# Kernel optimization log

Measured on AMD Instinct MI355X. Metric: run time of the kernel, lower is better.

The kernel has to match this reference:

```python
import jax, jax.numpy as jnp
import numpy as np

GRID = 128      # voxel grid extent per axis
NUM_BATCH = 4
N_PER = 25000   # points per scene (unique voxels)
C = 128
K = 32          # number of classes in probs
HEADS = 8
SCALE = 1.0


def setup_inputs() -> dict:
    key = jax.random.key(0)
    ks = jax.random.split(key, 12)
    N = NUM_BATCH * N_PER
    # unique voxel coordinates per scene (submanifold conv assumes no duplicate sites)
    coords_list = []
    for b in range(NUM_BATCH):
        flat = jax.random.permutation(jax.random.fold_in(ks[0], b), GRID ** 3)[:N_PER]
        xyz = jnp.stack([flat // (GRID * GRID), (flat // GRID) % GRID, flat % GRID], axis=1)
        bcol = jnp.full((N_PER, 1), b)
        coords_list.append(jnp.concatenate([bcol, xyz], axis=1))
    coords = jnp.concatenate(coords_list, axis=0).astype(jnp.int32)  # [N,4] = (b,x,y,z)
    feats = jax.random.normal(ks[1], (N, C), jnp.float32)
    probs = jax.random.normal(ks[2], (N, K), jnp.float32)
    conv_w = jax.random.normal(ks[3], (27, C, C), jnp.float32) * (1.0 / np.sqrt(27 * C))
    bn_gamma = 1.0 + 0.1 * jax.random.normal(ks[4], (C,), jnp.float32)
    bn_beta = 0.1 * jax.random.normal(ks[5], (C,), jnp.float32)
    in_proj_w = jax.random.normal(ks[6], (3 * C, C), jnp.float32) / np.sqrt(C)
    in_proj_b = 0.01 * jax.random.normal(ks[7], (3 * C,), jnp.float32)
    out_proj_w = jax.random.normal(ks[8], (C, C), jnp.float32) / np.sqrt(C)
    out_proj_b = 0.01 * jax.random.normal(ks[9], (C,), jnp.float32)
    bottleneck_w = jax.random.normal(ks[10], (C, 2 * C), jnp.float32) / np.sqrt(2 * C)
    return {"feats": feats, "probs": probs, "conv_w": conv_w, "bn_gamma": bn_gamma,
            "bn_beta": bn_beta, "in_proj_w": in_proj_w, "in_proj_b": in_proj_b,
            "out_proj_w": out_proj_w, "out_proj_b": out_proj_b,
            "bottleneck_w": bottleneck_w, "coords": coords, "batch_size": NUM_BATCH}


def _subm_conv3x3(feats, coords, conv_w, batch_size):
    """Submanifold 3x3x3 sparse conv: outputs only at active sites, gathering active neighbors."""
    N = feats.shape[0]
    b, xyz = coords[:, 0], coords[:, 1:]
    grid = jnp.full((batch_size, GRID, GRID, GRID), -1, jnp.int32)
    grid = grid.at[b, xyz[:, 0], xyz[:, 1], xyz[:, 2]].set(jnp.arange(N, dtype=jnp.int32))
    out = jnp.zeros((N, conv_w.shape[-1]), feats.dtype)
    kidx = 0
    for dx in (-1, 0, 1):
        for dy in (-1, 0, 1):
            for dz in (-1, 0, 1):
                nb = xyz + jnp.array([dx, dy, dz], jnp.int32)
                inb = jnp.all((nb >= 0) & (nb < GRID), axis=1)
                nbc = jnp.clip(nb, 0, GRID - 1)
                j = grid[b, nbc[:, 0], nbc[:, 1], nbc[:, 2]]
                ok = inb & (j >= 0)
                g = jnp.where(ok[:, None], feats[jnp.maximum(j, 0)], 0.0)
                out = out + g @ conv_w[kidx]
                kidx += 1
    return out


def _forward(feats, probs, conv_w, bn_gamma, bn_beta, in_proj_w, in_proj_b,
             out_proj_w, out_proj_b, bottleneck_w, coords, batch_size):
    N, Cc = feats.shape
    dh = Cc // HEADS
    b = coords[:, 0]
    # transform_input: SubMConv3d -> BatchNorm1d (batch stats) -> ReLU
    x = _subm_conv3x3(feats, coords, conv_w, batch_size)
    mu = jnp.mean(x, axis=0)
    var = jnp.var(x, axis=0)
    x = jax.nn.relu((x - mu) * jax.lax.rsqrt(var + 1e-5) * bn_gamma + bn_beta)
    # SpatialGatherModule: per-scene softmax over points, soft-weighted context [B,K,C]
    m = b[None, :] == jnp.arange(batch_size, dtype=b.dtype)[:, None]          # [B,N]
    neg = jnp.finfo(x.dtype).min
    z = jnp.where(m[:, :, None], (SCALE * probs)[None], neg)                  # [B,N,K]
    w = jax.nn.softmax(z, axis=1)
    ctx = jnp.einsum('bnk,nc->bkc', w, x)                                     # [B,K,C]
    # per-scene MultiheadAttention (unbatched): query = points, key/value = context
    Wq, Wk, Wv = in_proj_w[:Cc], in_proj_w[Cc:2 * Cc], in_proj_w[2 * Cc:]
    bq, bk, bv = in_proj_b[:Cc], in_proj_b[Cc:2 * Cc], in_proj_b[2 * Cc:]
    q = ((x @ Wq.T + bq) * (dh ** -0.5)).reshape(N, HEADS, dh)
    kh = (ctx @ Wk.T + bk).reshape(batch_size, -1, HEADS, dh)
    vh = (ctx @ Wv.T + bv).reshape(batch_size, -1, HEADS, dh)
    scores = jnp.einsum('nhd,bkhd->nbhk', q, kh)
    scores = scores[jnp.arange(N), b]                                         # [N,H,K] pick own scene
    attn = jax.nn.softmax(scores, axis=-1)
    o = jnp.einsum('nhk,bkhd->nbhd', attn, vh)[jnp.arange(N), b]              # [N,H,dh]
    attn_out = o.reshape(N, Cc) @ out_proj_w.T + out_proj_b
    # torch code aliases feats with inputs.features, so the in-place scatter makes
    # both halves of the concat equal to attn_out (literal forward semantics)
    y = jnp.concatenate([attn_out, attn_out], axis=1) @ bottleneck_w.T
    return y


def reference(feats, probs, conv_w, bn_gamma, bn_beta, in_proj_w, in_proj_b,
              out_proj_w, out_proj_b, bottleneck_w, coords, batch_size):
    return _forward(feats, probs, conv_w, bn_gamma, bn_beta, in_proj_w, in_proj_b,
                    out_proj_w, out_proj_b, bottleneck_w, coords, batch_size)
```

## Files before the change

### kernel.cpp

```cpp
#include <hip/hip_runtime.h>
#include <hip/hip_bf16.h>

typedef __attribute__((ext_vector_type(8))) short short8;
typedef __attribute__((ext_vector_type(4))) float floatx4;

#define NB 4
#define GRIDD 128
#define GRID3 (128*128*128)
#define C 128
#define KSLOT 32
#define CTX_BPB 256
#define DEN_BLK 1024
#define STAT_BLK 1024
#define PCAP 8192
#define PREP_BLKS 2048

static __device__ __forceinline__ unsigned short f2bf(float f){
  unsigned u = __builtin_bit_cast(unsigned, f);
  unsigned r = (u + 0x7FFFu + ((u >> 16) & 1u)) >> 16;
  return (unsigned short)r;
}
static __device__ __forceinline__ float bf2f(unsigned short h){
  unsigned u = ((unsigned)h) << 16;
  return __builtin_bit_cast(float, u);
}

__global__ void prepk(const float* __restrict__ feats, const float* __restrict__ convw,
                      const float* __restrict__ inw, const int* __restrict__ coords,
                      const float* __restrict__ bw, const float* __restrict__ outw,
                      const float* __restrict__ outb,
                      unsigned short* __restrict__ Fb, unsigned short* __restrict__ Wt,
                      unsigned short* __restrict__ Wq, unsigned short* __restrict__ WkvT,
                      int* __restrict__ gh, unsigned short* __restrict__ W2b,
                      float* __restrict__ b2, long total1)
{
  const int t = threadIdx.x;
  if (blockIdx.x >= PREP_BLKS){
    __shared__ float wcf[128];
    __shared__ float red[128];
    const int o = blockIdx.x - PREP_BLKS;
    if (t < 128){
      const float w_i = bw[(size_t)o*256 + t] + bw[(size_t)o*256 + 128 + t];
      wcf[t] = w_i;
      red[t] = w_i * outb[t];
    }
    __syncthreads();
    if (t < 128){
      float acc = 0.f;
      #pragma unroll 8
      for (int j = 0; j < 128; j++) acc = fmaf(wcf[j], outw[j*128 + t], acc);
      W2b[o*128 + t] = f2bf(acc);
    }
    for (int s = 64; s > 0; s >>= 1){
      if (t < s) red[t] += red[t + s];
      __syncthreads();
    }
    if (t == 0) b2[o] = red[0];
    return;
  }
  const long stride = (long)PREP_BLKS * blockDim.x;
  const long i0 = (long)blockIdx.x * blockDim.x + t;
  const long q4 = total1 >> 2;
  const float4* f4 = reinterpret_cast<const float4*>(feats);
  ushort4* fb4 = reinterpret_cast<ushort4*>(Fb);
  for (long i = i0; i < q4; i += stride){
    const float4 v = f4[i];
    ushort4 o; o.x = f2bf(v.x); o.y = f2bf(v.y); o.z = f2bf(v.z); o.w = f2bf(v.w);
    fb4[i] = o;
  }
  for (long i = i0; i < 27L*C*C; i += stride){
    long k = i >> 14; long r = (i >> 7) & 127; long c = i & 127;
    Wt[i] = f2bf(convw[(k << 14) + (c << 7) + r]);
  }
  for (long i = i0; i < C*C; i += stride) Wq[i] = f2bf(inw[i]);
  for (long i = i0; i < 2L*C*C; i += stride){
    long which = i >> 14, rem = i & 16383, ii = rem >> 7, cout = rem & 127;
    WkvT[i] = f2bf(inw[((1 + which) << 14) + (cout << 7) + ii]);
  }
  const long nsites = total1 >> 7;
  for (long i = i0; i < nsites; i += stride){
    const int4 cr = *reinterpret_cast<const int4*>(coords + i * 4);
    gh[(((cr.x*GRIDD + cr.y)*GRIDD + cr.z)*GRIDD) + cr.w] = (int)i;
  }
}

__global__ __launch_bounds__(256) void pairk(const int* __restrict__ coords,
                                             const int* __restrict__ gh,
                                             int2* __restrict__ pairs,
                                             int* __restrict__ gcnt, int N){
  __shared__ int wcnt[4][27];
  __shared__ int woff[4][27];
  const int t = threadIdx.x, wave = t >> 6, lane = t & 63;
  const int p = blockIdx.x * 256 + t;
  const bool active = p < N;
  int4 cr = make_int4(0, 0, 0, 0);
  if (active) cr = *reinterpret_cast<const int4*>(coords + (size_t)p * 4);
  const int b = cr.x, x = cr.y, y = cr.z, z = cr.w;
  int jl[27];
  #pragma unroll
  for (int k = 0; k < 27; k++){
    jl[k] = -1;
    if (k == 13) continue;
    if (active){
      const int dx = k / 9 - 1, dy = (k / 3) % 3 - 1, dz = k % 3 - 1;
      const int nx = x + dx, ny = y + dy, nz = z + dz;
      if (((unsigned)nx < 128u) & ((unsigned)ny < 128u) & ((unsigned)nz < 128u)){
        const int gi = ((((b << 7) + nx) << 7) + ny) * GRIDD + nz;
        const int jj = gh[gi];
        if ((unsigned)jj < (unsigned)N){
          const int4 cj = *reinterpret_cast<const int4*>(coords + (size_t)jj * 4);
          if (cj.x == b && cj.y == nx && cj.z == ny && cj.w == nz) jl[k] = jj;
        }
      }
    }
  }
  #pragma unroll
  for (int k = 0; k < 27; k++){
    const unsigned long long m = __ballot(jl[k] >= 0);
    if (lane == 0) wcnt[wave][k] = (int)__popcll(m);
  }
  __syncthreads();
  if (t < 27){
    const int c0 = wcnt[0][t], c1 = wcnt[1][t], c2 = wcnt[2][t], c3 = wcnt[3][t];
    const int tot = c0 + c1 + c2 + c3;
    int gb = 0;
    if (t != 13 && tot > 0) gb = atomicAdd(&gcnt[t], tot);
    woff[0][t] = gb;
    woff[1][t] = gb + c0;
    woff[2][t] = gb + c0 + c1;
    woff[3][t] = gb + c0 + c1 + c2;
  }
  __syncthreads();
  const unsigned long long ltm = ((unsigned long long)1 << lane) - 1;
  #pragma unroll
  for (int k = 0; k < 27; k++){
    if (k == 13) continue;
    const unsigned long long m = __ballot(jl[k] >= 0);
    if (jl[k] >= 0){
      const int slot = woff[wave][k] + (int)__popcll(m & ltm);
      if (slot < PCAP) pairs[(size_t)k * PCAP + slot] = make_int2(p, jl[k]);
    }
  }
}

__global__ __launch_bounds__(256) void scatk(
    const unsigned short* __restrict__ F, const unsigned short* __restrict__ Wt,
    const int2* __restrict__ pairs, const int* __restrict__ gcnt,
    float* __restrict__ X, int N)
{
  __shared__ unsigned short wl[128 * 136];
  const int k = (blockIdx.x < 13) ? blockIdx.x : blockIdx.x + 1;
  const int t = threadIdx.x;
  const unsigned short* wg = Wt + (size_t)k * C * C;
  for (int idx = t; idx < 128 * 16; idx += 256){
    const int row = idx >> 4, seg = idx & 15;
    *reinterpret_cast<short8*>(&wl[row * 136 + seg * 8]) =
        *reinterpret_cast<const short8*>(wg + row * 128 + seg * 8);
  }
  __syncthreads();
  const int cnt = min(gcnt[k], PCAP);
  const int nch = (cnt + 15) >> 4;
  const int wave = t >> 6, lane = t & 63, lo = lane & 15, hi = lane >> 4;
  for (int c = blockIdx.y * 4 + wave; c < nch; c += 32 * 4){
    const int pidx = c * 16 + lo;
    const bool pv = pidx < cnt;
    const int2 pr = pv ? pairs[(size_t)k * PCAP + pidx] : make_int2(0, 0);
    const unsigned short* frow = F + (size_t)pr.y * C;
    short8 a[4];
    #pragma unroll
    for (int kc = 0; kc < 4; kc++){
      a[kc] = *reinterpret_cast<const short8*>(frow + kc * 32 + hi * 8);
      if (!pv) a[kc] = (short8){0,0,0,0,0,0,0,0};
    }
    floatx4 acc[8];
    #pragma unroll
    for (int i = 0; i < 8; i++) acc[i] = (floatx4){0.f,0.f,0.f,0.f};
    #pragma unroll
    for (int kc = 0; kc < 4; kc++){
      const int koff = kc * 32 + hi * 8;
      #pragma unroll
      for (int ct = 0; ct < 8; ct++){
        const short8 b = *reinterpret_cast<const short8*>(&wl[(ct*16 + lo) * 136 + koff]);
        acc[ct] = __builtin_amdgcn_mfma_f32_16x16x32_bf16(a[kc], b, acc[ct], 0, 0, 0);
      }
    }
    #pragma unroll
    for (int i2 = 0; i2 < 4; i2++){
      const int src = hi * 4 + i2;
      const int row = __shfl(pr.x, src);
      if (c * 16 + src < cnt){
        #pragma unroll
        for (int ct = 0; ct < 8; ct++)
          atomicAdd(&X[(size_t)row * C + ct * 16 + lo], acc[ct][i2]);
      }
    }
  }
}

__global__ __launch_bounds__(256) void sdk(const float* __restrict__ X,
                                           const float* __restrict__ probs,
                                           const int* __restrict__ coords,
                                           float* __restrict__ spgs,
                                           float* __restrict__ dpart, int N){
  __shared__ float ls[256][4];
  __shared__ float lq[256][4];
  const int t = threadIdx.x;
  if (blockIdx.x < STAT_BLK){
    const int blk = blockIdx.x;
    const int c4 = t & 31, rg = t >> 5;
    float s0=0.f,s1=0.f,s2=0.f,s3=0.f, q0=0.f,q1=0.f,q2=0.f,q3=0.f;
    for (int r = blk * 8 + rg; r < N; r += STAT_BLK * 8){
      const float4 v = *reinterpret_cast<const float4*>(X + (size_t)r * C + c4 * 4);
      s0 += v.x; s1 += v.y; s2 += v.z; s3 += v.w;
      q0 = fmaf(v.x, v.x, q0); q1 = fmaf(v.y, v.y, q1);
      q2 = fmaf(v.z, v.z, q2); q3 = fmaf(v.w, v.w, q3);
    }
    ls[t][0]=s0; ls[t][1]=s1; ls[t][2]=s2; ls[t][3]=s3;
    lq[t][0]=q0; lq[t][1]=q1; lq[t][2]=q2; lq[t][3]=q3;
    __syncthreads();
    if (t < 32){
      float as[4]={0.f,0.f,0.f,0.f}, aq[4]={0.f,0.f,0.f,0.f};
      #pragma unroll
      for (int g = 0; g < 8; g++){
        #pragma unroll
        for (int j = 0; j < 4; j++){ as[j] += ls[g*32 + t][j]; aq[j] += lq[g*32 + t][j]; }
      }
      #pragma unroll
      for (int j = 0; j < 4; j++){
        spgs[(size_t)blk * 256 + t*4 + j] = as[j];
        spgs[(size_t)blk * 256 + 128 + t*4 + j] = aq[j];
      }
    }
  } else {
    const int blk = blockIdx.x - STAT_BLK;
    const int k = t & 31, rh = t >> 5;
    float a0 = 0.f, a1 = 0.f, a2 = 0.f, a3 = 0.f;
    for (int r = blk * 8 + rh; r < N; r += DEN_BLK * 8){
      const int b = coords[(size_t)r * 4];
      const float e = __expf(probs[(size_t)r * 32 + k]);
      a0 += (b == 0) ? e : 0.f;
      a1 += (b == 1) ? e : 0.f;
      a2 += (b == 2) ? e : 0.f;
      a3 += (b == 3) ? e : 0.f;
    }
    float (*dls)[128] = reinterpret_cast<float (*)[128]>(&ls[0][0]);
    dls[rh][0*32 + k] = a0; dls[rh][1*32 + k] = a1;
    dls[rh][2*32 + k] = a2; dls[rh][3*32 + k] = a3;
    __syncthreads();
    if (t < 128){
      float s = 0.f;
      #pragma unroll
      for (int j = 0; j < 8; j++) s += dls[j][t];
      dpart[(size_t)blk * 128 + t] = s;
    }
  }
}

__global__ __launch_bounds__(128) void reduk(const float* __restrict__ pgs,
                                             const float* __restrict__ dpart,
                                             float* __restrict__ gsum,
                                             float* __restrict__ gsq,
                                             float* __restrict__ denom){
  const int which = blockIdx.x, slice = blockIdx.y, t = threadIdx.x;
  float s = 0.f;
  if (which < 2){
    const float* src = pgs + which * 128 + t;
    for (int j = slice; j < STAT_BLK; j += 8) s += src[(size_t)j * 256];
    atomicAdd((which ? gsq : gsum) + t, s);
  } else {
    const float* src = dpart + t;
    for (int j = slice; j < DEN_BLK; j += 8) s += src[(size_t)j * 128];
    atomicAdd(denom + t, s);
  }
}

__global__ void finalizek(const float* __restrict__ sums, const float* __restrict__ sumsq,
                          const float* __restrict__ gamma, const float* __restrict__ beta,
                          const float* __restrict__ denom,
                          float* __restrict__ scalev, float* __restrict__ shiftv,
                          float* __restrict__ invden, int N){
  const int t = threadIdx.x;
  const float invN = 1.f / (float)N;
  const float mu = sums[t] * invN;
  const float var = sumsq[t] * invN - mu * mu;
  const float sc = gamma[t] * rsqrtf(var + 1e-5f);
  scalev[t] = sc;
  shiftv[t] = beta[t] - mu * sc;
  invden[t] = 1.f / denom[t];
}

__global__ __launch_bounds__(256) void ctx2k(const float* __restrict__ Xm,
                                             const float* __restrict__ probs,
                                             const float* __restrict__ scalev,
                                             const float* __restrict__ shiftv,
                                             float* __restrict__ pbuf,
                                             unsigned short* __restrict__ xb, int NPER){
  __shared__ float xL[32 * 128];
  __shared__ float pe[32 * 32];
  __shared__ float red[2 * KSLOT * C];
  __shared__ float scL[128], shL[128];
  const int blk = blockIdx.x;
  const int b = blk >> 8, j = blk & 255;
  const int rows = (NPER + CTX_BPB - 1) / CTX_BPB;
  const int r0 = j * rows;
  const int r1 = min(r0 + rows, NPER);
  const int t = threadIdx.x, c = t & 127, rh = t >> 7;
  if (t < 128){ scL[t] = scalev[t]; shL[t] = shiftv[t]; }
  __syncthreads();
  const float sc = scL[c], sh = shL[c];
  float acc[KSLOT];
  #pragma unroll
  for (int k = 0; k < KSLOT; k++) acc[k] = 0.f;

  const int wr = t >> 3;
  const int wc = (t & 7) * 16;

  for (int base = r0; base < r1; base += 32){
    __syncthreads();
    #pragma unroll
    for (int i = 0; i < 4; i++){
      const int idx = i * 256 + t;
      const int r = idx >> 5, c4 = idx & 31;
      const int rr = base + r;
      float4 v = make_float4(0.f, 0.f, 0.f, 0.f);
      if (rr < r1) v = *reinterpret_cast<const float4*>(Xm + ((size_t)b * NPER + rr) * C + c4 * 4);
      *reinterpret_cast<float4*>(&xL[r * 128 + c4 * 4]) = v;
    }
    {
      const int r = t >> 3, k4 = t & 7;
      const int rr = base + r;
      float4 v = make_float4(0.f, 0.f, 0.f, 0.f);
      if (rr < r1){
        const float4 pv = *reinterpret_cast<const float4*>(probs + ((size_t)b * NPER + rr) * 32 + k4 * 4);
        v.x = __expf(pv.x); v.y = __expf(pv.y); v.z = __expf(pv.z); v.w = __expf(pv.w);
      }
      *reinterpret_cast<float4*>(&pe[r * 32 + k4 * 4]) = v;
    }
    __syncthreads();
    {
      const int rr = base + wr;
      if (rr < r1){
        short8 o0, o1;
        #pragma unroll
        for (int jj = 0; jj < 8; jj++){
          o0[jj] = (short)f2bf(fmaxf(fmaf(xL[wr * 128 + wc + jj], scL[wc + jj], shL[wc + jj]), 0.f));
          o1[jj] = (short)f2bf(fmaxf(fmaf(xL[wr * 128 + wc + 8 + jj], scL[wc + 8 + jj], shL[wc + 8 + jj]), 0.f));
        }
        unsigned short* xp = xb + ((size_t)b * NPER + rr) * C + wc;
        *reinterpret_cast<short8*>(xp) = o0;
        *reinterpret_cast<short8*>(xp + 8) = o1;
      }
    }
    const int rend = min(32, r1 - base);
    for (int r = rh; r < rend; r += 2){
      const float xv = fmaxf(fmaf(xL[r * 128 + c], sc, sh), 0.f);
      const float4* wrp = reinterpret_cast<const float4*>(&pe[r * 32]);
      #pragma unroll
      for (int kq = 0; kq < 8; kq++){
        const float4 w4 = wrp[kq];
        acc[kq*4+0] = fmaf(w4.x, xv, acc[kq*4+0]);
        acc[kq*4+1] = fmaf(w4.y, xv, acc[kq*4+1]);
        acc[kq*4+2] = fmaf(w4.z, xv, acc[kq*4+2]);
        acc[kq*4+3] = fmaf(w4.w, xv, acc[kq*4+3]);
      }
    }
  }
  __syncthreads();
  #pragma unroll
  for (int k = 0; k < KSLOT; k++) red[(rh * KSLOT + k) * C + c] = acc[k];
  __syncthreads();
  float* dst = pbuf + (size_t)blk * KSLOT * C;
  for (int i = t; i < KSLOT * C; i += 256) dst[i] = red[i] + red[KSLOT * C + i];
}

__global__ __launch_bounds__(256) void kvk(const float* __restrict__ pbuf,
                                           const float* __restrict__ invden,
                                           const unsigned short* __restrict__ WkvT,
                                           const float* __restrict__ inb,
                                           float* __restrict__ kh, float* __restrict__ vh){
  __shared__ float rowp[2][C];
  __shared__ float row[C];
  const int bk = blockIdx.x;
  const int b = bk >> 5, k = bk & 31;
  const int t = threadIdx.x, c = t & 127, jh = t >> 7;
  float s = 0.f;
  for (int j = jh; j < CTX_BPB; j += 2)
    s += pbuf[((size_t)(b * CTX_BPB + j) * KSLOT + k) * C + c];
  rowp[jh][c] = s;
  __syncthreads();
  if (t < C) row[t] = (rowp[0][t] + rowp[1][t]) * invden[b * KSLOT + k];
  __syncthreads();
  const int which = t >> 7;
  const unsigned short* W = WkvT + (size_t)which * C * C;
  float acc = inb[(1 + which) * C + c];
  #pragma unroll 8
  for (int i = 0; i < C; i++) acc = fmaf(row[i], bf2f(W[i * C + c]), acc);
  (which ? vh : kh)[(size_t)bk * C + c] = acc;
}

__global__ __launch_bounds__(256) void gemm128(
    const unsigned short* __restrict__ A, const unsigned short* __restrict__ W,
    const float* __restrict__ bias, float scale,
    float* __restrict__ outF, unsigned short* __restrict__ outB, int N)
{
  const int tid = threadIdx.x;
  const int wave = tid >> 6, lane = tid & 63;
  const int rbase = blockIdx.x * 64 + (wave >> 1) * 32;
  const int cbase = (wave & 1) * 64;
  const int lo = lane & 15, hi = lane >> 4;
  floatx4 acc[2][4];
  #pragma unroll
  for (int rt = 0; rt < 2; rt++)
    #pragma unroll
    for (int ct = 0; ct < 4; ct++) acc[rt][ct] = (floatx4){0.f,0.f,0.f,0.f};
  const int m0 = rbase + lo, m1 = rbase + 16 + lo;
  const int m0c = m0 < N ? m0 : N - 1;
  const int m1c = m1 < N ? m1 : N - 1;
  #pragma unroll
  for (int kc = 0; kc < 4; kc++){
    const int koff = kc * 32 + hi * 8;
    const short8 a0 = *reinterpret_cast<const short8*>(A + (size_t)m0c * C + koff);
    const short8 a1 = *reinterpret_cast<const short8*>(A + (size_t)m1c * C + koff);
    #pragma unroll
    for (int ct = 0; ct < 4; ct++){
      const int n = cbase + ct * 16 + lo;
      const short8 b = *reinterpret_cast<const short8*>(W + (size_t)n * C + koff);
      acc[0][ct] = __builtin_amdgcn_mfma_f32_16x16x32_bf16(b, a0, acc[0][ct], 0, 0, 0);
      acc[1][ct] = __builtin_amdgcn_mfma_f32_16x16x32_bf16(b, a1, acc[1][ct], 0, 0, 0);
    }
  }
  #pragma unroll
  for (int rt = 0; rt < 2; rt++){
    const int row = rbase + rt * 16 + lo;
    if (row < N){
      #pragma unroll
      for (int ct = 0; ct < 4; ct++){
        const int col = cbase + ct * 16 + hi * 4;
        float4 bv = make_float4(0.f, 0.f, 0.f, 0.f);
        if (bias) bv = *reinterpret_cast<const float4*>(bias + col);
        float4 v;
        v.x = (acc[rt][ct][0] + bv.x) * scale;
        v.y = (acc[rt][ct][1] + bv.y) * scale;
        v.z = (acc[rt][ct][2] + bv.z) * scale;
        v.w = (acc[rt][ct][3] + bv.w) * scale;
        if (outF) *reinterpret_cast<float4*>(outF + (size_t)row * C + col) = v;
        if (outB){
          ushort4 u;
          u.x = f2bf(v.x); u.y = f2bf(v.y); u.z = f2bf(v.z); u.w = f2bf(v.w);
          *reinterpret_cast<ushort4*>(outB + (size_t)row * C + col) = u;
        }
      }
    }
  }
}

__global__ __launch_bounds__(256) void attn5k(const unsigned short* __restrict__ qb,
                                              const float* __restrict__ kh,
                                              const float* __restrict__ vh,
                                              unsigned short* __restrict__ ob, int NPER){
  __shared__ float khL[KSLOT * C];
  __shared__ float vhL[KSLOT * C];
  const int t = threadIdx.x;
  const int b = blockIdx.y;
  const int n0 = blockIdx.x * 64;
  {
    const float4* ks = reinterpret_cast<const float4*>(kh + (size_t)b * KSLOT * C);
    const float4* vs = reinterpret_cast<const float4*>(vh + (size_t)b * KSLOT * C);
    float4* kd = reinterpret_cast<float4*>(khL);
    float4* vd = reinterpret_cast<float4*>(vhL);
    #pragma unroll
    for (int i = 0; i < 4; i++){ kd[i * 256 + t] = ks[i * 256 + t]; vd[i * 256 + t] = vs[i * 256 + t]; }
  }
  __syncthreads();
  const int h = t >> 5, p = t & 31;
  const int na = n0 + p, nb = n0 + 32 + p;
  const int nac = na < NPER ? na : NPER - 1;
  const int nbc = nb < NPER ? nb : NPER - 1;
  float qa[16], qc[16];
  {
    const short8* qpa = reinterpret_cast<const short8*>(qb + ((size_t)b * NPER + nac) * C + h * 16);
    const short8* qpb = reinterpret_cast<const short8*>(qb + ((size_t)b * NPER + nbc) * C + h * 16);
    const short8 a0 = qpa[0], a1 = qpa[1];
    const short8 b0 = qpb[0], b1 = qpb[1];
    #pragma unroll
    for (int i = 0; i < 8; i++){
      qa[i]     = bf2f((unsigned short)a0[i]);
      qa[8 + i] = bf2f((unsigned short)a1[i]);
      qc[i]     = bf2f((unsigned short)b0[i]);
      qc[8 + i] = bf2f((unsigned short)b1[i]);
    }
  }
  float ma = -3.0e38f, mb = -3.0e38f;
  float sa = 0.f, sb = 0.f;
  float oa[16], oc[16];
  #pragma unroll
  for (int i = 0; i < 16; i++){ oa[i] = 0.f; oc[i] = 0.f; }
  for (int tau = 0; tau < 4; tau++){
    float va[8], vb[8];
    #pragma unroll
    for (int kk = 0; kk < 8; kk++){
      const int k = tau * 8 + kk;
      const float4* kp = reinterpret_cast<const float4*>(&khL[k * C + h * 16]);
      const float4 k0 = kp[0], k1 = kp[1], k2 = kp[2], k3 = kp[3];
      float x, y;
      x = qa[0] * k0.x;            y = qc[0] * k0.x;
      x = fmaf(qa[1],  k0.y, x);   y = fmaf(qc[1],  k0.y, y);
      x = fmaf(qa[2],  k0.z, x);   y = fmaf(qc[2],  k0.z, y);
      x = fmaf(qa[3],  k0.w, x);   y = fmaf(qc[3],  k0.w, y);
      x = fmaf(qa[4],  k1.x, x);   y = fmaf(qc[4],  k1.x, y);
      x = fmaf(qa[5],  k1.y, x);   y = fmaf(qc[5],  k1.y, y);
      x = fmaf(qa[6],  k1.z, x);   y = fmaf(qc[6],  k1.z, y);
      x = fmaf(qa[7],  k1.w, x);   y = fmaf(qc[7],  k1.w, y);
      x = fmaf(qa[8],  k2.x, x);   y = fmaf(qc[8],  k2.x, y);
      x = fmaf(qa[9],  k2.y, x);   y = fmaf(qc[9],  k2.y, y);
      x = fmaf(qa[10], k2.z, x);   y = fmaf(qc[10], k2.z, y);
      x = fmaf(qa[11], k2.w, x);   y = fmaf(qc[11], k2.w, y);
      x = fmaf(qa[12], k3.x, x);   y = fmaf(qc[12], k3.x, y);
      x = fmaf(qa[13], k3.y, x);   y = fmaf(qc[13], k3.y, y);
      x = fmaf(qa[14], k3.z, x);   y = fmaf(qc[14], k3.z, y);
      x = fmaf(qa[15], k3.w, x);   y = fmaf(qc[15], k3.w, y);
      va[kk] = x; vb[kk] = y;
    }
    float tma = va[0], tmb = vb[0];
    #pragma unroll
    for (int kk = 1; kk < 8; kk++){ tma = fmaxf(tma, va[kk]); tmb = fmaxf(tmb, vb[kk]); }
    const float ma2 = fmaxf(ma, tma), mb2 = fmaxf(mb, tmb);
    const float fa = __expf(ma - ma2), fb = __expf(mb - mb2);
    ma = ma2; mb = mb2;
    sa *= fa; sb *= fb;
    #pragma unroll
    for (int i = 0; i < 16; i++){ oa[i] *= fa; oc[i] *= fb; }
    #pragma unroll
    for (int kk = 0; kk < 8; kk++){
      const float ea = __expf(va[kk] - ma);
      const float eb = __expf(vb[kk] - mb);
      va[kk] = ea; vb[kk] = eb;
      sa += ea; sb += eb;
    }
    #pragma unroll
    for (int kk = 0; kk < 8; kk++){
      const int k = tau * 8 + kk;
      const float4* vp = reinterpret_cast<const float4*>(&vhL[k * C + h * 16]);
      const float4 v0 = vp[0], v1 = vp[1], v2 = vp[2], v3 = vp[3];
      const float wa = va[kk], wb = vb[kk];
      oa[0]  = fmaf(wa, v0.x, oa[0]);   oc[0]  = fmaf(wb, v0.x, oc[0]);
      oa[1]  = fmaf(wa, v0.y, oa[1]);   oc[1]  = fmaf(wb, v0.y, oc[1]);
      oa[2]  = fmaf(wa, v0.z, oa[2]);   oc[2]  = fmaf(wb, v0.z, oc[2]);
      oa[3]  = fmaf(wa, v0.w, oa[3]);   oc[3]  = fmaf(wb, v0.w, oc[3]);
      oa[4]  = fmaf(wa, v1.x, oa[4]);   oc[4]  = fmaf(wb, v1.x, oc[4]);
      oa[5]  = fmaf(wa, v1.y, oa[5]);   oc[5]  = fmaf(wb, v1.y, oc[5]);
      oa[6]  = fmaf(wa, v1.z, oa[6]);   oc[6]  = fmaf(wb, v1.z, oc[6]);
      oa[7]  = fmaf(wa, v1.w, oa[7]);   oc[7]  = fmaf(wb, v1.w, oc[7]);
      oa[8]  = fmaf(wa, v2.x, oa[8]);   oc[8]  = fmaf(wb, v2.x, oc[8]);
      oa[9]  = fmaf(wa, v2.y, oa[9]);   oc[9]  = fmaf(wb, v2.y, oc[9]);
      oa[10] = fmaf(wa, v2.z, oa[10]);  oc[10] = fmaf(wb, v2.z, oc[10]);
      oa[11] = fmaf(wa, v2.w, oa[11]);  oc[11] = fmaf(wb, v2.w, oc[11]);
      oa[12] = fmaf(wa, v3.x, oa[12]);  oc[12] = fmaf(wb, v3.x, oc[12]);
      oa[13] = fmaf(wa, v3.y, oa[13]);  oc[13] = fmaf(wb, v3.y, oc[13]);
      oa[14] = fmaf(wa, v3.z, oa[14]);  oc[14] = fmaf(wb, v3.z, oc[14]);
      oa[15] = fmaf(wa, v3.w, oa[15]);  oc[15] = fmaf(wb, v3.w, oc[15]);
    }
  }
  const float inva = 1.f / sa, invb = 1.f / sb;
  if (na < NPER){
    short8 s0, s1;
    #pragma unroll
    for (int i = 0; i < 8; i++){
      s0[i] = (short)f2bf(oa[i] * inva);
      s1[i] = (short)f2bf(oa[8 + i] * inva);
    }
    unsigned short* op = ob + ((size_t)b * NPER + na) * C + h * 16;
    *reinterpret_cast<short8*>(op) = s0;
    *reinterpret_cast<short8*>(op + 8) = s1;
  }
  if (nb < NPER){
    short8 s0, s1;
    #pragma unroll
    for (int i = 0; i < 8; i++){
      s0[i] = (short)f2bf(oc[i] * invb);
      s1[i] = (short)f2bf(oc[8 + i] * invb);
    }
    unsigned short* op = ob + ((size_t)b * NPER + nb) * C + h * 16;
    *reinterpret_cast<short8*>(op) = s0;
    *reinterpret_cast<short8*>(op + 8) = s1;
  }
}

extern "C" void kernel_launch(void* const* d_in, const int* in_sizes, int n_in,
                              void* d_out, int out_size, void* d_ws, size_t ws_size,
                              hipStream_t stream){
  const float* feats  = (const float*)d_in[0];
  const float* probs  = (const float*)d_in[1];
  const float* convw  = (const float*)d_in[2];
  const float* gamma  = (const float*)d_in[3];
  const float* beta   = (const float*)d_in[4];
  const float* inw    = (const float*)d_in[5];
  const float* inb    = (const float*)d_in[6];
  const float* outw   = (const float*)d_in[7];
  const float* outb   = (const float*)d_in[8];
  const float* bw     = (const float*)d_in[9];
  const int*   coords = (const int*)d_in[10];
  const int N = in_sizes[0] / C;
  const int NPER = N / NB;
  const int NBLK = (N + 63) / 64;

  char* ws = (char*)d_ws;
  size_t off = 0;
  auto alloc = [&](size_t bytes) -> char* {
    char* r = ws + off; off += (bytes + 255) & ~(size_t)255; return r;
  };
  int* grid_h            = (int*)alloc((size_t)NB * GRID3 * 4);
  unsigned short* featsb = (unsigned short*)alloc((size_t)N * C * 2);
  unsigned short* convwt = (unsigned short*)alloc((size_t)27 * C * C * 2);
  unsigned short* wq     = (unsigned short*)alloc((size_t)C * C * 2);
  unsigned short* wkvT   = (unsigned short*)alloc((size_t)2 * C * C * 2);
  unsigned short* w2b    = (unsigned short*)alloc((size_t)C * C * 2);
  float* b2              = (float*)alloc(512);
  float* xconv           = (float*)alloc((size_t)N * C * 4);
  unsigned short* qb     = (unsigned short*)alloc((size_t)N * C * 2);
  unsigned short* xb     = (unsigned short*)alloc((size_t)N * C * 2);
  int2* pairs            = (int2*)alloc((size_t)27 * PCAP * 8);
  float* spgs            = (float*)alloc((size_t)STAT_BLK * 256 * 4);
  float* dpart           = (float*)alloc((size_t)DEN_BLK * 128 * 4);
  float* zero_base       = (float*)alloc((size_t)512 * 4);
  float* gsum   = zero_base;
  float* gsq    = zero_base + 128;
  float* denom  = zero_base + 256;
  int*   gcnt   = (int*)(zero_base + 384);
  float* invden = (float*)alloc(512);
  float* scalev = (float*)alloc(512);
  float* shiftv = (float*)alloc(512);
  float* kh     = (float*)alloc((size_t)NB * KSLOT * C * 4);
  float* vh     = (float*)alloc((size_t)NB * KSLOT * C * 4);
  float* pbuf = (float*)grid_h;
  unsigned short* o_bf = featsb;

  (void)hipMemsetAsync(zero_base, 0, (size_t)512 * 4, stream);
  prepk<<<PREP_BLKS + 128, 256, 0, stream>>>(feats, convw, inw, coords, bw, outw, outb,
                                             featsb, convwt, wq, wkvT, grid_h, w2b, b2,
                                             (long)N * C);
  pairk<<<(N + 255) / 256, 256, 0, stream>>>(coords, grid_h, pairs, gcnt, N);
  gemm128<<<NBLK, 256, 0, stream>>>(featsb, convwt + 13 * C * C, nullptr, 1.f, xconv, nullptr, N);
  scatk<<<dim3(26, 32), 256, 0, stream>>>(featsb, convwt, pairs, gcnt, xconv, N);
  sdk<<<STAT_BLK + DEN_BLK, 256, 0, stream>>>(xconv, probs, coords, spgs, dpart, N);
  {
    dim3 rg(3, 8);
    reduk<<<rg, 128, 0, stream>>>(spgs, dpart, gsum, gsq, denom);
  }
  finalizek<<<1, 128, 0, stream>>>(gsum, gsq, gamma, beta, denom, scalev, shiftv, invden, N);
  ctx2k<<<NB * CTX_BPB, 256, 0, stream>>>(xconv, probs, scalev, shiftv, pbuf, xb, NPER);
  kvk<<<NB * KSLOT, 256, 0, stream>>>(pbuf, invden, wkvT, inb, kh, vh);
  gemm128<<<NBLK, 256, 0, stream>>>(xb, wq, inb, 0.25f, nullptr, qb, N);
  dim3 agrid((NPER + 63) / 64, NB);
  attn5k<<<agrid, 256, 0, stream>>>(qb, kh, vh, o_bf, NPER);
  gemm128<<<NBLK, 256, 0, stream>>>(o_bf, w2b, b2, 1.f, (float*)d_out, nullptr, N);
}
```

Measured before the change: 428.0 us.

## Fuse Q projection into attention, softmax denominator into ctx, finalize into reduce

Computes the Q projection inside the attention kernel with MFMA into shared memory, which removes a separate GEMM launch and the qb round-trip through global memory. The softmax-denominator partials now come from exp(probs) values already loaded in ctx2k, so sdk no longer re-reads probs and coords. Separately, the BN finalize step is folded into the reduction kernel using a last-block counter, which drops one launch. In exchange, attention blocks now do extra GEMM work and read the Q weights directly from global memory, and kvk gains a tree reduction.

```diff
diff --git a/kernel.cpp b/kernel.cpp
--- a/kernel.cpp
+++ b/kernel.cpp
@@ -10,7 +10,6 @@
 #define C 128
 #define KSLOT 32
 #define CTX_BPB 256
-#define DEN_BLK 1024
 #define STAT_BLK 1024
 #define PCAP 8192
 #define PREP_BLKS 2048
@@ -198,95 +197,65 @@
 }
 
 __global__ __launch_bounds__(256) void sdk(const float* __restrict__ X,
-                                           const float* __restrict__ probs,
-                                           const int* __restrict__ coords,
-                                           float* __restrict__ spgs,
-                                           float* __restrict__ dpart, int N){
+                                           float* __restrict__ spgs, int N){
   __shared__ float ls[256][4];
   __shared__ float lq[256][4];
   const int t = threadIdx.x;
-  if (blockIdx.x < STAT_BLK){
-    const int blk = blockIdx.x;
-    const int c4 = t & 31, rg = t >> 5;
-    float s0=0.f,s1=0.f,s2=0.f,s3=0.f, q0=0.f,q1=0.f,q2=0.f,q3=0.f;
-    for (int r = blk * 8 + rg; r < N; r += STAT_BLK * 8){
-      const float4 v = *reinterpret_cast<const float4*>(X + (size_t)r * C + c4 * 4);
-      s0 += v.x; s1 += v.y; s2 += v.z; s3 += v.w;
-      q0 = fmaf(v.x, v.x, q0); q1 = fmaf(v.y, v.y, q1);
-      q2 = fmaf(v.z, v.z, q2); q3 = fmaf(v.w, v.w, q3);
-    }
-    ls[t][0]=s0; ls[t][1]=s1; ls[t][2]=s2; ls[t][3]=s3;
-    lq[t][0]=q0; lq[t][1]=q1; lq[t][2]=q2; lq[t][3]=q3;
-    __syncthreads();
-    if (t < 32){
-      float as[4]={0.f,0.f,0.f,0.f}, aq[4]={0.f,0.f,0.f,0.f};
+  const int blk = blockIdx.x;
+  const int c4 = t & 31, rg = t >> 5;
+  float s0=0.f,s1=0.f,s2=0.f,s3=0.f, q0=0.f,q1=0.f,q2=0.f,q3=0.f;
+  for (int r = blk * 8 + rg; r < N; r += STAT_BLK * 8){
+    const float4 v = *reinterpret_cast<const float4*>(X + (size_t)r * C + c4 * 4);
+    s0 += v.x; s1 += v.y; s2 += v.z; s3 += v.w;
+    q0 = fmaf(v.x, v.x, q0); q1 = fmaf(v.y, v.y, q1);
+    q2 = fmaf(v.z, v.z, q2); q3 = fmaf(v.w, v.w, q3);
+  }
+  ls[t][0]=s0; ls[t][1]=s1; ls[t][2]=s2; ls[t][3]=s3;
+  lq[t][0]=q0; lq[t][1]=q1; lq[t][2]=q2; lq[t][3]=q3;
+  __syncthreads();
+  if (t < 32){
+    float as[4]={0.f,0.f,0.f,0.f}, aq[4]={0.f,0.f,0.f,0.f};
+    #pragma unroll
+    for (int g = 0; g < 8; g++){
       #pragma unroll
-      for (int g = 0; g < 8; g++){
-        #pragma unroll
-        for (int j = 0; j < 4; j++){ as[j] += ls[g*32 + t][j]; aq[j] += lq[g*32 + t][j]; }
-      }
-      #pragma unroll
-      for (int j = 0; j < 4; j++){
-        spgs[(size_t)blk * 256 + t*4 + j] = as[j];
-        spgs[(size_t)blk * 256 + 128 + t*4 + j] = aq[j];
-      }
-    }
-  } else {
-    const int blk = blockIdx.x - STAT_BLK;
-    const int k = t & 31, rh = t >> 5;
-    float a0 = 0.f, a1 = 0.f, a2 = 0.f, a3 = 0.f;
-    for (int r = blk * 8 + rh; r < N; r += DEN_BLK * 8){
-      const int b = coords[(size_t)r * 4];
-      const float e = __expf(probs[(size_t)r * 32 + k]);
-      a0 += (b == 0) ? e : 0.f;
-      a1 += (b == 1) ? e : 0.f;
-      a2 += (b == 2) ? e : 0.f;
-      a3 += (b == 3) ? e : 0.f;
-    }
-    float (*dls)[128] = reinterpret_cast<float (*)[128]>(&ls[0][0]);
-    dls[rh][0*32 + k] = a0; dls[rh][1*32 + k] = a1;
-    dls[rh][2*32 + k] = a2; dls[rh][3*32 + k] = a3;
-    __syncthreads();
-    if (t < 128){
-      float s = 0.f;
-      #pragma unroll
-      for (int j = 0; j < 8; j++) s += dls[j][t];
-      dpart[(size_t)blk * 128 + t] = s;
+      for (int j = 0; j < 4; j++){ as[j] += ls[g*32 + t][j]; aq[j] += lq[g*32 + t][j]; }
+    }
+    #pragma unroll
+    for (int j = 0; j < 4; j++){
+      spgs[(size_t)blk * 256 + t*4 + j] = as[j];
+      spgs[(size_t)blk * 256 + 128 + t*4 + j] = aq[j];
     }
   }
 }
 
 __global__ __launch_bounds__(128) void reduk(const float* __restrict__ pgs,
-                                             const float* __restrict__ dpart,
                                              float* __restrict__ gsum,
                                              float* __restrict__ gsq,
-                                             float* __restrict__ denom){
+                                             const float* __restrict__ gamma,
+                                             const float* __restrict__ beta,
+                                             float* __restrict__ scalev,
+                                             float* __restrict__ shiftv,
+                                             int* __restrict__ cnt, int N){
   const int which = blockIdx.x, slice = blockIdx.y, t = threadIdx.x;
+  const float* src = pgs + which * 128 + t;
   float s = 0.f;
-  if (which < 2){
-    const float* src = pgs + which * 128 + t;
-    for (int j = slice; j < STAT_BLK; j += 8) s += src[(size_t)j * 256];
-    atomicAdd((which ? gsq : gsum) + t, s);
-  } else {
-    const float* src = dpart + t;
-    for (int j = slice; j < DEN_BLK; j += 8) s += src[(size_t)j * 128];
-    atomicAdd(denom + t, s);
-  }
-}
-
-__global__ void finalizek(const float* __restrict__ sums, const float* __restrict__ sumsq,
-                          const float* __restrict__ gamma, const float* __restrict__ beta,
-                          const float* __restrict__ denom,
-                          float* __restrict__ scalev, float* __restrict__ shiftv,
-                          float* __restrict__ invden, int N){
-  const int t = threadIdx.x;
-  const float invN = 1.f / (float)N;
-  const float mu = sums[t] * invN;
-  const float var = sumsq[t] * invN - mu * mu;
-  const float sc = gamma[t] * rsqrtf(var + 1e-5f);
-  scalev[t] = sc;
-  shiftv[t] = beta[t] - mu * sc;
-  invden[t] = 1.f / denom[t];
+  for (int j = slice; j < STAT_BLK; j += 8) s += src[(size_t)j * 256];
+  atomicAdd((which ? gsq : gsum) + t, s);
+  __threadfence();
+  __syncthreads();
+  __shared__ int last;
+  if (t == 0) last = (atomicAdd(cnt, 1) == 15);
+  __syncthreads();
+  if (last){
+    const float gs = atomicAdd(gsum + t, 0.f);
+    const float gq = atomicAdd(gsq + t, 0.f);
+    const float invN = 1.f / (float)N;
+    const float mu = gs * invN;
+    const float var = gq * invN - mu * mu;
+    const float sc = gamma[t] * rsqrtf(var + 1e-5f);
+    scalev[t] = sc;
+    shiftv[t] = beta[t] - mu * sc;
+  }
 }
 
 __global__ __launch_bounds__(256) void ctx2k(const float* __restrict__ Xm,
@@ -294,7 +263,8 @@
                                              const float* __restrict__ scalev,
                                              const float* __restrict__ shiftv,
                                              float* __restrict__ pbuf,
-                                             unsigned short* __restrict__ xb, int NPER){
+                                             unsigned short* __restrict__ xb,
+                                             float* __restrict__ dpart2, int NPER){
   __shared__ float xL[32 * 128];
   __shared__ float pe[32 * 32];
   __shared__ float red[2 * KSLOT * C];
@@ -311,6 +281,8 @@
   float acc[KSLOT];
   #pragma unroll
   for (int k = 0; k < KSLOT; k++) acc[k] = 0.f;
+  const int dk = t & 31, dg = t >> 5;
+  float dsum = 0.f;
 
   const int wr = t >> 3;
   const int wc = (t & 7) * 16;
@@ -351,6 +323,8 @@
         *reinterpret_cast<short8*>(xp + 8) = o1;
       }
     }
+    #pragma unroll
+    for (int rr4 = 0; rr4 < 4; rr4++) dsum += pe[(dg + rr4 * 8) * 32 + dk];
     const int rend = min(32, r1 - base);
     for (int r = rh; r < rend; r += 2){
       const float xv = fmaxf(fmaf(xL[r * 128 + c], sc, sh), 0.f);
@@ -368,27 +342,41 @@
   __syncthreads();
   #pragma unroll
   for (int k = 0; k < KSLOT; k++) red[(rh * KSLOT + k) * C + c] = acc[k];
+  pe[dg * 32 + dk] = dsum;
   __syncthreads();
   float* dst = pbuf + (size_t)blk * KSLOT * C;
   for (int i = t; i < KSLOT * C; i += 256) dst[i] = red[i] + red[KSLOT * C + i];
+  if (t < 32){
+    float s = 0.f;
+    #pragma unroll
+    for (int g = 0; g < 8; g++) s += pe[g * 32 + t];
+    dpart2[(size_t)t * (NB * CTX_BPB) + blk] = s;
+  }
 }
 
 __global__ __launch_bounds__(256) void kvk(const float* __restrict__ pbuf,
-                                           const float* __restrict__ invden,
+                                           const float* __restrict__ dpart2,
                                            const unsigned short* __restrict__ WkvT,
                                            const float* __restrict__ inb,
                                            float* __restrict__ kh, float* __restrict__ vh){
   __shared__ float rowp[2][C];
   __shared__ float row[C];
+  __shared__ float dred[256];
   const int bk = blockIdx.x;
   const int b = bk >> 5, k = bk & 31;
   const int t = threadIdx.x, c = t & 127, jh = t >> 7;
+  dred[t] = dpart2[(size_t)k * (NB * CTX_BPB) + b * CTX_BPB + t];
   float s = 0.f;
   for (int j = jh; j < CTX_BPB; j += 2)
     s += pbuf[((size_t)(b * CTX_BPB + j) * KSLOT + k) * C + c];
   rowp[jh][c] = s;
   __syncthreads();
-  if (t < C) row[t] = (rowp[0][t] + rowp[1][t]) * invden[b * KSLOT + k];
+  for (int sred = 128; sred > 0; sred >>= 1){
+    if (t < sred) dred[t] += dred[t + sred];
+    __syncthreads();
+  }
+  const float invden = 1.f / dred[0];
+  if (t < C) row[t] = (rowp[0][t] + rowp[1][t]) * invden;
   __syncthreads();
   const int which = t >> 7;
   const unsigned short* W = WkvT + (size_t)which * C * C;
@@ -454,12 +442,15 @@
   }
 }
 
-__global__ __launch_bounds__(256) void attn5k(const unsigned short* __restrict__ qb,
+__global__ __launch_bounds__(256) void attn6k(const unsigned short* __restrict__ xb,
+                                              const unsigned short* __restrict__ wq,
+                                              const float* __restrict__ inb,
                                               const float* __restrict__ kh,
                                               const float* __restrict__ vh,
                                               unsigned short* __restrict__ ob, int NPER){
   __shared__ float khL[KSLOT * C];
   __shared__ float vhL[KSLOT * C];
+  __shared__ unsigned short qL[64 * 136];
   const int t = threadIdx.x;
   const int b = blockIdx.y;
   const int n0 = blockIdx.x * 64;
@@ -471,15 +462,55 @@
     #pragma unroll
     for (int i = 0; i < 4; i++){ kd[i * 256 + t] = ks[i * 256 + t]; vd[i * 256 + t] = vs[i * 256 + t]; }
   }
+  const int wave = t >> 6, lane = t & 63;
+  const int rb = (wave >> 1) * 32, cb = (wave & 1) * 64;
+  const int lo = lane & 15, hi = lane >> 4;
+  {
+    floatx4 qa2[2][4];
+    #pragma unroll
+    for (int rt = 0; rt < 2; rt++)
+      #pragma unroll
+      for (int ct = 0; ct < 4; ct++) qa2[rt][ct] = (floatx4){0.f,0.f,0.f,0.f};
+    const unsigned short* A = xb + (size_t)b * NPER * C;
+    const int m0 = n0 + rb + lo, m1 = n0 + rb + 16 + lo;
+    const int m0c = m0 < NPER ? m0 : NPER - 1;
+    const int m1c = m1 < NPER ? m1 : NPER - 1;
+    #pragma unroll
+    for (int kc = 0; kc < 4; kc++){
+      const int koff = kc * 32 + hi * 8;
+      const short8 a0 = *reinterpret_cast<const short8*>(A + (size_t)m0c * C + koff);
+      const short8 a1 = *reinterpret_cast<const short8*>(A + (size_t)m1c * C + koff);
+      #pragma unroll
+      for (int ct = 0; ct < 4; ct++){
+        const int n = cb + ct * 16 + lo;
+        const short8 w = *reinterpret_cast<const short8*>(wq + (size_t)n * C + koff);
+        qa2[0][ct] = __builtin_amdgcn_mfma_f32_16x16x32_bf16(w, a0, qa2[0][ct], 0, 0, 0);
+        qa2[1][ct] = __builtin_amdgcn_mfma_f32_16x16x32_bf16(w, a1, qa2[1][ct], 0, 0, 0);
+      }
+    }
+    #pragma unroll
+    for (int rt = 0; rt < 2; rt++){
+      const int row = rb + rt * 16 + lo;
+      #pragma unroll
+      for (int ct = 0; ct < 4; ct++){
+        const int col = cb + ct * 16 + hi * 4;
+        const float4 bv = *reinterpret_cast<const float4*>(inb + col);
+        ushort4 u;
+        u.x = f2bf((qa2[rt][ct][0] + bv.x) * 0.25f);
+        u.y = f2bf((qa2[rt][ct][1] + bv.y) * 0.25f);
+        u.z = f2bf((qa2[rt][ct][2] + bv.z) * 0.25f);
+        u.w = f2bf((qa2[rt][ct][3] + bv.w) * 0.25f);
+        *reinterpret_cast<ushort4*>(&qL[row * 136 + col]) = u;
+      }
+    }
+  }
   __syncthreads();
   const int h = t >> 5, p = t & 31;
-  const int na = n0 + p, nb = n0 + 32 + p;
-  const int nac = na < NPER ? na : NPER - 1;
-  const int nbc = nb < NPER ? nb : NPER - 1;
+  const int na = n0 + p, nb2 = n0 + 32 + p;
   float qa[16], qc[16];
   {
-    const short8* qpa = reinterpret_cast<const short8*>(qb + ((size_t)b * NPER + nac) * C + h * 16);
-    const short8* qpb = reinterpret_cast<const short8*>(qb + ((size_t)b * NPER + nbc) * C + h * 16);
+    const short8* qpa = reinterpret_cast<const short8*>(&qL[p * 136 + h * 16]);
+    const short8* qpb = reinterpret_cast<const short8*>(&qL[(32 + p) * 136 + h * 16]);
     const short8 a0 = qpa[0], a1 = qpa[1];
     const short8 b0 = qpb[0], b1 = qpb[1];
     #pragma unroll
@@ -573,14 +604,14 @@
     *reinterpret_cast<short8*>(op) = s0;
     *reinterpret_cast<short8*>(op + 8) = s1;
   }
-  if (nb < NPER){
+  if (nb2 < NPER){
     short8 s0, s1;
     #pragma unroll
     for (int i = 0; i < 8; i++){
       s0[i] = (short)f2bf(oc[i] * invb);
       s1[i] = (short)f2bf(oc[8 + i] * invb);
     }
-    unsigned short* op = ob + ((size_t)b * NPER + nb) * C + h * 16;
+    unsigned short* op = ob + ((size_t)b * NPER + nb2) * C + h * 16;
     *reinterpret_cast<short8*>(op) = s0;
     *reinterpret_cast<short8*>(op + 8) = s1;
   }
@@ -617,17 +648,15 @@
   unsigned short* w2b    = (unsigned short*)alloc((size_t)C * C * 2);
   float* b2              = (float*)alloc(512);
   float* xconv           = (float*)alloc((size_t)N * C * 4);
-  unsigned short* qb     = (unsigned short*)alloc((size_t)N * C * 2);
   unsigned short* xb     = (unsigned short*)alloc((size_t)N * C * 2);
   int2* pairs            = (int2*)alloc((size_t)27 * PCAP * 8);
   float* spgs            = (float*)alloc((size_t)STAT_BLK * 256 * 4);
-  float* dpart           = (float*)alloc((size_t)DEN_BLK * 128 * 4);
+  float* dpart2          = (float*)alloc((size_t)32 * NB * CTX_BPB * 4);
   float* zero_base       = (float*)alloc((size_t)512 * 4);
   float* gsum   = zero_base;
   float* gsq    = zero_base + 128;
-  float* denom  = zero_base + 256;
-  int*   gcnt   = (int*)(zero_base + 384);
-  float* invden = (float*)alloc(512);
+  int*   gcnt   = (int*)(zero_base + 256);
+  int*   cnt    = (int*)(zero_base + 384);
   float* scalev = (float*)alloc(512);
   float* shiftv = (float*)alloc(512);
   float* kh     = (float*)alloc((size_t)NB * KSLOT * C * 4);
@@ -642,16 +671,14 @@
   pairk<<<(N + 255) / 256, 256, 0, stream>>>(coords, grid_h, pairs, gcnt, N);
   gemm128<<<NBLK, 256, 0, stream>>>(featsb, convwt + 13 * C * C, nullptr, 1.f, xconv, nullptr, N);
   scatk<<<dim3(26, 32), 256, 0, stream>>>(featsb, convwt, pairs, gcnt, xconv, N);
-  sdk<<<STAT_BLK + DEN_BLK, 256, 0, stream>>>(xconv, probs, coords, spgs, dpart, N);
+  sdk<<<STAT_BLK, 256, 0, stream>>>(xconv, spgs, N);
   {
-    dim3 rg(3, 8);
-    reduk<<<rg, 128, 0, stream>>>(spgs, dpart, gsum, gsq, denom);
-  }
-  finalizek<<<1, 128, 0, stream>>>(gsum, gsq, gamma, beta, denom, scalev, shiftv, invden, N);
-  ctx2k<<<NB * CTX_BPB, 256, 0, stream>>>(xconv, probs, scalev, shiftv, pbuf, xb, NPER);
-  kvk<<<NB * KSLOT, 256, 0, stream>>>(pbuf, invden, wkvT, inb, kh, vh);
-  gemm128<<<NBLK, 256, 0, stream>>>(xb, wq, inb, 0.25f, nullptr, qb, N);
+    dim3 rg(2, 8);
+    reduk<<<rg, 128, 0, stream>>>(spgs, gsum, gsq, gamma, beta, scalev, shiftv, cnt, N);
+  }
+  ctx2k<<<NB * CTX_BPB, 256, 0, stream>>>(xconv, probs, scalev, shiftv, pbuf, xb, dpart2, NPER);
+  kvk<<<NB * KSLOT, 256, 0, stream>>>(pbuf, dpart2, wkvT, inb, kh, vh);
   dim3 agrid((NPER + 63) / 64, NB);
-  attn5k<<<agrid, 256, 0, stream>>>(qb, kh, vh, o_bf, NPER);
+  attn6k<<<agrid, 256, 0, stream>>>(xb, wq, inb, kh, vh, o_bf, NPER);
   gemm128<<<NBLK, 256, 0, stream>>>(o_bf, w2b, b2, 1.f, (float*)d_out, nullptr, N);
 }
```

New measurement: 418.4 us, median of 2. -2.3%, faster.
